# Performance work log

Hardware: AMD Instinct MI355X
Metric: run time of the kernel (lower is better)

## Reference

```python
import jax, jax.numpy as jnp
import numpy as np

EPS = 1e-5
WSZ = 8
DH = 32


def _ln_chan(x, g, b):
    # channel LayerNorm over dim=1 of (B,C,H,W), biased variance
    mu = jnp.mean(x, axis=1, keepdims=True)
    var = jnp.mean((x - mu) ** 2, axis=1, keepdims=True)
    return (x - mu) / jnp.sqrt(var + EPS) * g[None, :, None, None] + b[None, :, None, None]


def _conv_transpose2d(x, w, b, stride, pad):
    # torch ConvTranspose2d: w is (C_in, C_out, kh, kw)
    k = w.shape[2]
    wf = jnp.flip(w, (2, 3)).transpose(1, 0, 2, 3)  # (O, I, kh, kw)
    out = jax.lax.conv_general_dilated(
        x, wf, window_strides=(1, 1),
        padding=[(k - 1 - pad, k - 1 - pad)] * 2,
        lhs_dilation=(stride, stride),
        dimension_numbers=("NCHW", "OIHW", "NCHW"))
    return out + b[None, :, None, None]


def _rope_cs(wh, ww, dh, dtype):
    quarter = dh // 4
    freq = 1.0 / (10000.0 ** (jnp.arange(quarter, dtype=dtype) / quarter))
    th = jnp.arange(wh, dtype=dtype)[:, None] * freq          # (wh, q)
    tw = jnp.arange(ww, dtype=dtype)[:, None] * freq          # (ww, q)
    th = jnp.broadcast_to(th[:, None, :], (wh, ww, quarter)).reshape(wh * ww, quarter)
    tw = jnp.broadcast_to(tw[None, :, :], (wh, ww, quarter)).reshape(wh * ww, quarter)
    theta = jnp.concatenate([th, tw], axis=-1)                # (L, dh/2)
    cos = jnp.concatenate([jnp.cos(theta), jnp.cos(theta)], axis=-1)  # (L, dh)
    sin = jnp.concatenate([jnp.sin(theta), jnp.sin(theta)], axis=-1)
    return cos, sin


def _rot_half(x):
    x1, x2 = jnp.split(x, 2, axis=-1)
    return jnp.concatenate([-x2, x1], axis=-1)


def _attn_block(x, g, b, wqkv, wout, bout, shifted):
    B, C, H, W = x.shape
    heads = C // DH
    xn = _ln_chan(x, g, b)
    if shifted:
        xn = jnp.roll(xn, shift=(-(WSZ // 2), -(WSZ // 2)), axis=(2, 3))
    nh, nw = H // WSZ, W // WSZ
    # window partition: (B,C,H,W) -> (B*nh*nw, L, C), L = WSZ*WSZ
    t = xn.reshape(B, C, nh, WSZ, nw, WSZ).transpose(0, 2, 4, 3, 5, 1)
    t = t.reshape(B * nh * nw, WSZ * WSZ, C)
    qkv = t @ wqkv.T                                           # (Bw, L, 3C)
    q, k, v = jnp.split(qkv, 3, axis=-1)

    def split_heads(a):
        return a.reshape(a.shape[0], a.shape[1], heads, DH).transpose(0, 2, 1, 3)
    q, k, v = map(split_heads, (q, k, v))                      # (Bw, h, L, d)
    cos, sin = _rope_cs(WSZ, WSZ, DH, q.dtype)                 # (L, d)
    q = q * cos + _rot_half(q) * sin
    k = k * cos + _rot_half(k) * sin
    scale = DH ** -0.5
    att = jax.nn.softmax(jnp.einsum("bhid,bhjd->bhij", q * scale, k), axis=-1)
    out = jnp.einsum("bhij,bhjd->bhid", att, v)                # (Bw, h, L, d)
    out = out.transpose(0, 2, 1, 3).reshape(B * nh * nw, WSZ * WSZ, C)
    out = out @ wout.T + bout
    out = out.reshape(B, nh, nw, WSZ, WSZ, C).transpose(0, 5, 1, 3, 2, 4).reshape(B, C, H, W)
    if shifted:
        out = jnp.roll(out, shift=(WSZ // 2, WSZ // 2), axis=(2, 3))
    return out


def _ff(x, g, b, w1, b1, w2, b2):
    xn = _ln_chan(x, g, b)
    h = jnp.einsum("bchw,oc->bohw", xn, w1) + b1[None, :, None, None]
    h = jax.nn.gelu(h)
    return jnp.einsum("bchw,oc->bohw", h, w2) + b2[None, :, None, None]


def _forward(x, ct_w2, ct_b2, ct_w4, ct_b4,
             a1_g, a1_b, a1_wqkv, a1_wout, a1_bout,
             f1_g, f1_b, f1_w1, f1_b1, f1_w2, f1_b2,
             a2_g, a2_b, a2_wqkv, a2_wout, a2_bout,
             f2_g, f2_b, f2_w1, f2_b1, f2_w2, f2_b2):
    # CrossExpandLayer: kernels [2,4], stride 2, padding (k-2)//2
    y2 = _conv_transpose2d(x, ct_w2, ct_b2, stride=2, pad=0)
    y4 = _conv_transpose2d(x, ct_w4, ct_b4, stride=2, pad=1)
    h = jnp.concatenate([y2, y4], axis=1)                      # (B, dim_out, 2H, 2W)
    h = h + _attn_block(h, a1_g, a1_b, a1_wqkv, a1_wout, a1_bout, shifted=False)
    h = h + _ff(h, f1_g, f1_b, f1_w1, f1_b1, f1_w2, f1_b2)
    h = h + _attn_block(h, a2_g, a2_b, a2_wqkv, a2_wout, a2_bout, shifted=True)
    h = h + _ff(h, f2_g, f2_b, f2_w1, f2_b1, f2_w2, f2_b2)
    return h


def setup_inputs() -> dict:
    key = jax.random.key(0)
    ks = jax.random.split(key, 32)
    DIM_IN, DIM = 512, 256
    MULT = 4
    s = 0.02
    inp = {"x": jax.random.normal(ks[0], (2, DIM_IN, 64, 128), dtype=jnp.float32)}
    # CrossExpandLayer: dim_scales = [128, 128]
    inp["ct_w2"] = jax.random.normal(ks[1], (DIM_IN, DIM // 2, 2, 2), jnp.float32) * s
    inp["ct_b2"] = jnp.zeros((DIM // 2,), jnp.float32)
    inp["ct_w4"] = jax.random.normal(ks[2], (DIM_IN, DIM // 2, 4, 4), jnp.float32) * s
    inp["ct_b4"] = jnp.zeros((DIM // 2,), jnp.float32)
    for i, pre in enumerate(["a1", "a2"]):
        inp[pre + "_g"] = jnp.ones((DIM,), jnp.float32)
        inp[pre + "_b"] = jnp.zeros((DIM,), jnp.float32)
        inp[pre + "_wqkv"] = jax.random.normal(ks[3 + 2 * i], (3 * DIM, DIM), jnp.float32) * s
        inp[pre + "_wout"] = jax.random.normal(ks[4 + 2 * i], (DIM, DIM), jnp.float32) * s
        inp[pre + "_bout"] = jnp.zeros((DIM,), jnp.float32)
    for i, pre in enumerate(["f1", "f2"]):
        inp[pre + "_g"] = jnp.ones((DIM,), jnp.float32)
        inp[pre + "_b"] = jnp.zeros((DIM,), jnp.float32)
        inp[pre + "_w1"] = jax.random.normal(ks[10 + 2 * i], (MULT * DIM, DIM), jnp.float32) * s
        inp[pre + "_b1"] = jnp.zeros((MULT * DIM,), jnp.float32)
        inp[pre + "_w2"] = jax.random.normal(ks[11 + 2 * i], (DIM, MULT * DIM), jnp.float32) * s
        inp[pre + "_b2"] = jnp.zeros((DIM,), jnp.float32)
    return inp


def reference(x, ct_w2, ct_b2, ct_w4, ct_b4,
              a1_g, a1_b, a1_wqkv, a1_wout, a1_bout,
              f1_g, f1_b, f1_w1, f1_b1, f1_w2, f1_b2,
              a2_g, a2_b, a2_wqkv, a2_wout, a2_bout,
              f2_g, f2_b, f2_w1, f2_b1, f2_w2, f2_b2):
    return _forward(x, ct_w2, ct_b2, ct_w4, ct_b4,
                    a1_g, a1_b, a1_wqkv, a1_wout, a1_bout,
                    f1_g, f1_b, f1_w1, f1_b1, f1_w2, f1_b2,
                    a2_g, a2_b, a2_wqkv, a2_wout, a2_bout,
                    f2_g, f2_b, f2_w1, f2_b1, f2_w2, f2_b2)
```

## Files before the change

kernel.cpp:

```cpp
#include <hip/hip_runtime.h>
#include <hip/hip_bf16.h>
#include <math.h>

typedef __bf16 bf16_t;
typedef __bf16 bf16x8 __attribute__((ext_vector_type(8)));
typedef float  f32x4 __attribute__((ext_vector_type(4)));

constexpr int B_  = 2;
constexpr int CIN = 512, HI = 64, WI = 128;
constexpr int C_  = 256, H_ = 128, W_ = 256;
constexpr int NTOK = B_ * H_ * W_;
constexpr int NWIN = 1024;

__device__ __forceinline__ unsigned short f2bu(float x) {
    return __builtin_bit_cast(unsigned short, (bf16_t)x);
}

__global__ __launch_bounds__(256) void k_rope(float* __restrict__ rope) {
    int i = blockIdx.x * 256 + threadIdx.x;
    if (i >= 2048) return;
    int l = i >> 5, d = i & 31;
    int j = d & 15;
    int ly = l >> 3, lx = l & 7;
    float fr = powf(10000.f, -(float)(j & 7) / 8.f);
    float t = (j < 8 ? (float)ly : (float)lx) * fr;
    rope[i]        = cosf(t);
    rope[2048 + i] = sinf(t);
}

struct CvtSeg { const float* s; bf16_t* d; unsigned n; };
struct CvtParams { CvtSeg seg[8]; };

__global__ __launch_bounds__(256) void k_cvt(CvtParams P) {
    unsigned base = (blockIdx.x * 256u + threadIdx.x) * 4u;
    for (int s = 0; s < 8; s++) {
        unsigned n = P.seg[s].n;
        if (base < n) {
            float4 v = *(const float4*)(P.seg[s].s + base);
            ushort4 o;
            o.x = f2bu(v.x); o.y = f2bu(v.y); o.z = f2bu(v.z); o.w = f2bu(v.w);
            *(ushort4*)(P.seg[s].d + base) = o;
            return;
        }
        base -= n;
    }
}

__global__ __launch_bounds__(256) void k_trx(const float* __restrict__ x,
                                             bf16_t* __restrict__ xT) {
    __shared__ float t[64][65];
    int pos0 = blockIdx.x << 6;
    int ci0  = blockIdx.y << 6;
    int b    = blockIdx.z;
    int tid = threadIdx.x;
    int cpos = tid & 63, rb = tid >> 6;
    const float* src = x + ((size_t)(b * CIN + ci0) << 13) + pos0;
    #pragma unroll
    for (int i = 0; i < 16; i++) {
        int ci = rb + (i << 2);
        t[ci][cpos] = src[((size_t)ci << 13) + cpos];
    }
    __syncthreads();
    int row = tid >> 2, q = tid & 3;
    bf16_t* dst = xT + ((size_t)((b << 13) + pos0 + row) << 9) + ci0 + (q << 4);
    union { uint4 u[2]; unsigned short us[16]; } o;
    #pragma unroll
    for (int e = 0; e < 16; e++)
        o.us[e] = f2bu(t[(q << 4) + e][row]);
    *(uint4*)dst = o.u[0];
    *(uint4*)(dst + 8) = o.u[1];
}

__global__ __launch_bounds__(256) void k_bmat(const float* __restrict__ w2,
                                              const float* __restrict__ w4,
                                              const float* __restrict__ cb2,
                                              const float* __restrict__ cb4,
                                              bf16_t* __restrict__ B512,
                                              bf16_t* __restrict__ B2048,
                                              float* __restrict__ cbias) {
    int idx = blockIdx.x * 256 + threadIdx.x;
    if (idx < 262144) {
        int ci = idx & 511, o = (idx >> 9) & 127, p = idx >> 16;
        int rp = p >> 1, rq = p & 1;
        B512[idx] = (bf16_t)w2[((ci * 128 + o) * 2 + rp) * 2 + rq];
        if (idx < 256) cbias[idx] = idx < 128 ? cb2[idx] : cb4[idx - 128];
    } else {
        int i4 = idx - 262144;
        int k = i4 & 2047, o2 = (i4 >> 11) & 127, p = i4 >> 18;
        int ci = k & 511, t = k >> 9;
        int rp = p >> 1, rq = p & 1, a = t >> 1, c = t & 1;
        int kh = 3 - rp - 2 * a, kw = 3 - rq - 2 * c;
        B2048[i4] = (bf16_t)w4[((ci * 128 + o2) * 4 + kh) * 4 + kw];
    }
}

__device__ __forceinline__ int winmap_pos(int idx, int shift) {
    int win = idx >> 6, l = idx & 63;
    int b = win >> 9, wy = (win >> 5) & 15, wx = win & 31;
    int y = ((wy << 3) + (l >> 3) + shift) & 127;
    int x = ((wx << 3) + (l & 7) + shift) & 255;
    return (b << 15) + (y << 8) + x;
}

__device__ __forceinline__ float gelu_tanh(float x) {
    float u = 1.5957691216057308f * (x + 0.044715f * x * x * x);
    return x - x * __builtin_amdgcn_rcpf(__expf(u) + 1.f);
}

__device__ __forceinline__ int swz(int row, int byteoff) {
    return (row << 7) + (byteoff ^ ((row & 7) << 4));
}

template<int MODE>
__device__ __forceinline__ void gemm_body(
    char* smem,
    const bf16_t* __restrict__ A, const bf16_t* __restrict__ Bw,
    const float* __restrict__ bias, bf16_t* __restrict__ Cb,
    float* __restrict__ Hres, const float* __restrict__ rope,
    int K, int ldc, int pshift, int colbase)
{
    char* Asb = smem;
    char* Bsb = smem + 16384;
    const int tid = threadIdx.x;

    int gx = gridDim.x;
    int bx = blockIdx.x, by = blockIdx.y;
    if ((gridDim.y & 7) == 0) {
        int lin = by * gx + bx;
        int grp = gx << 3;
        int q = lin / grp, r = lin - q * grp;
        by = (r & 7) + (q << 3);
        bx = r >> 3;
    }
    const int m0 = by << 7, n0 = bx << 7;

    const int w = tid >> 6, l = tid & 63;
    const int wm = (w >> 1) << 6, wn = (w & 1) << 6;
    const int r16 = l & 15, r4 = l >> 4;
    const int arow = tid >> 3, abyte = (tid & 7) << 4;

    const bf16_t* Ag = A + (size_t)(m0 + arow) * K + ((tid & 7) << 3);
    const bf16_t* Bg = Bw + (size_t)(n0 + arow) * K + ((tid & 7) << 3);

    f32x4 acc[4][4] = {};
    uint4 ra[4], rb[4];
    #pragma unroll
    for (int i = 0; i < 4; i++) {
        ra[i] = *(const uint4*)(Ag + (size_t)(i << 5) * K);
        rb[i] = *(const uint4*)(Bg + (size_t)(i << 5) * K);
    }
    for (int kt = 0; kt < K; kt += 64) {
        __syncthreads();
        #pragma unroll
        for (int i = 0; i < 4; i++) {
            *(uint4*)(Asb + swz(arow + (i << 5), abyte)) = ra[i];
            *(uint4*)(Bsb + swz(arow + (i << 5), abyte)) = rb[i];
        }
        __syncthreads();
        if (kt + 64 < K) {
            #pragma unroll
            for (int i = 0; i < 4; i++) {
                ra[i] = *(const uint4*)(Ag + (size_t)(i << 5) * K + kt + 64);
                rb[i] = *(const uint4*)(Bg + (size_t)(i << 5) * K + kt + 64);
            }
        }
        #pragma unroll
        for (int kk = 0; kk < 2; kk++) {
            bf16x8 af[4], bfr[4];
            #pragma unroll
            for (int f = 0; f < 4; f++)
                af[f] = *(const bf16x8*)(Asb + swz(wm + (f << 4) + r16, (kk << 6) + (r4 << 4)));
            #pragma unroll
            for (int f = 0; f < 4; f++)
                bfr[f] = *(const bf16x8*)(Bsb + swz(wn + (f << 4) + r16, (kk << 6) + (r4 << 4)));
            #pragma unroll
            for (int fm = 0; fm < 4; fm++)
                #pragma unroll
                for (int fn = 0; fn < 4; fn++)
                    acc[fm][fn] = __builtin_amdgcn_mfma_f32_16x16x32_bf16(
                        af[fm], bfr[fn], acc[fm][fn], 0, 0, 0);
        }
    }

    float* Lt = (float*)smem;
    const int wgrp = wn >> 6;
    #pragma unroll
    for (int p2 = 0; p2 < 2; p2++) {
        __syncthreads();
        if (wgrp == p2) {
            #pragma unroll
            for (int fm = 0; fm < 4; fm++) {
                int lrow = wm + (fm << 4) + (r4 << 2);
                #pragma unroll
                for (int fn = 0; fn < 4; fn++) {
                    f32x4 v = acc[fm][fn];
                    int lcol = (fn << 4) + r16;
                    #pragma unroll
                    for (int j = 0; j < 4; j++)
                        Lt[(lrow + j) * 72 + lcol] = v[j];
                }
            }
        }
        __syncthreads();
        if constexpr (MODE == 0) {
            const int c0 = (tid & 7) << 3;
            const int gcol = n0 + (p2 << 6) + c0;
            const int which = gcol >> 8;
            const int dbase = c0 & 31;
            const int pc = c0 ^ 16;
            const float sc = (which == 0) ? 0.17677669529663687f : 1.f;
            #pragma unroll
            for (int rnd = 0; rnd < 4; rnd++) {
                int row = (tid >> 3) + (rnd << 5);
                int lidx = (m0 + row) & 63;
                float vv[8];
                *(float4*)(vv)     = *(const float4*)(Lt + row * 72 + c0);
                *(float4*)(vv + 4) = *(const float4*)(Lt + row * 72 + c0 + 4);
                union { uint4 q; unsigned short us[8]; } o;
                if (which < 2) {
                    float pp[8];
                    *(float4*)(pp)     = *(const float4*)(Lt + row * 72 + pc);
                    *(float4*)(pp + 4) = *(const float4*)(Lt + row * 72 + pc + 4);
                    #pragma unroll
                    for (int i = 0; i < 8; i++) {
                        int d = dbase + i;
                        float cs = rope[lidx * 32 + d];
                        float sn = rope[2048 + lidx * 32 + d];
                        float rot = (d < 16) ? -pp[i] : pp[i];
                        o.us[i] = f2bu((vv[i] * cs + rot * sn) * sc);
                    }
                } else {
                    #pragma unroll
                    for (int i = 0; i < 8; i++) o.us[i] = f2bu(vv[i]);
                }
                *(uint4*)(Cb + (size_t)(m0 + row) * ldc + gcol) = o.q;
            }
        } else {
            const int c0 = (tid & 15) << 2;
            const int gcol = colbase + n0 + (p2 << 6) + c0;
            float bb[4];
            *(float4*)bb = *(const float4*)(bias + gcol);
            const int rp = pshift >> 1, rq = pshift & 1;
            #pragma unroll
            for (int rnd = 0; rnd < 8; rnd++) {
                int row = (tid >> 4) + (rnd << 4);
                float4 v = *(const float4*)(Lt + row * 72 + c0);
                int idx = m0 + row;
                int b = idx >> 13, u = (idx >> 7) & 63, vpos = idx & 127;
                int pos = (b << 15) + (((u << 1) + rp) << 8) + (vpos << 1) + rq;
                float* hp = Hres + ((size_t)pos << 8) + gcol;
                float4 r2;
                r2.x = v.x + bb[0]; r2.y = v.y + bb[1];
                r2.z = v.z + bb[2]; r2.w = v.w + bb[3];
                *(float4*)hp = r2;
            }
        }
    }
}

__device__ __forceinline__ void conv4_body(
    char* smem, const bf16_t* __restrict__ xT,
    const bf16_t* __restrict__ B2048, const float* __restrict__ cbias,
    float* __restrict__ h_t, int par)
{
    char* Asb = smem;
    char* Bsb = smem + 16384;
    const int tid = threadIdx.x;
    const int rp = par >> 1, rq = par & 1;
    const int m0 = blockIdx.y << 7;

    const int w = tid >> 6, l = tid & 63;
    const int wm = (w >> 1) << 6, wn = (w & 1) << 6;
    const int r16 = l & 15, r4 = l >> 4;
    const int arow = tid >> 3, abyte = (tid & 7) << 4;
    const int klane = (tid & 7) << 3;

    int mr_[4], u_[4], v_[4];
    #pragma unroll
    for (int i = 0; i < 4; i++) {
        mr_[i] = m0 + arow + (i << 5);
        u_[i] = (mr_[i] >> 7) & 63;
        v_[i] = mr_[i] & 127;
    }
    const bf16_t* Bp = B2048 + ((size_t)par << 18);

    auto loadA = [&](int c, uint4* r) {
        int t = c >> 3, ci0 = (c & 7) << 6;
        int dh = rp - 1 + (t >> 1), dw = rq - 1 + (t & 1);
        int off = (dh << 7) + dw;
        #pragma unroll
        for (int i = 0; i < 4; i++) {
            bool ok = ((unsigned)(u_[i] + dh) < (unsigned)HI) &&
                      ((unsigned)(v_[i] + dw) < (unsigned)WI);
            if (ok)
                r[i] = *(const uint4*)(xT + ((size_t)(mr_[i] + off) << 9) + ci0 + klane);
            else
                r[i] = uint4{0, 0, 0, 0};
        }
    };
    auto loadB = [&](int c, uint4* r) {
        #pragma unroll
        for (int i = 0; i < 4; i++)
            r[i] = *(const uint4*)(Bp + ((size_t)(arow + (i << 5)) << 11)
                                   + (c << 6) + klane);
    };

    f32x4 acc[4][4] = {};
    uint4 ra[4], rb[4];
    loadA(0, ra);
    loadB(0, rb);
    for (int c = 0; c < 32; c++) {
        __syncthreads();
        #pragma unroll
        for (int i = 0; i < 4; i++) {
            *(uint4*)(Asb + swz(arow + (i << 5), abyte)) = ra[i];
            *(uint4*)(Bsb + swz(arow + (i << 5), abyte)) = rb[i];
        }
        __syncthreads();
        if (c + 1 < 32) {
            loadA(c + 1, ra);
            loadB(c + 1, rb);
        }
        #pragma unroll
        for (int kk = 0; kk < 2; kk++) {
            bf16x8 af[4], bfr[4];
            #pragma unroll
            for (int f = 0; f < 4; f++)
                af[f] = *(const bf16x8*)(Asb + swz(wm + (f << 4) + r16, (kk << 6) + (r4 << 4)));
            #pragma unroll
            for (int f = 0; f < 4; f++)
                bfr[f] = *(const bf16x8*)(Bsb + swz(wn + (f << 4) + r16, (kk << 6) + (r4 << 4)));
            #pragma unroll
            for (int fm = 0; fm < 4; fm++)
                #pragma unroll
                for (int fn = 0; fn < 4; fn++)
                    acc[fm][fn] = __builtin_amdgcn_mfma_f32_16x16x32_bf16(
                        af[fm], bfr[fn], acc[fm][fn], 0, 0, 0);
        }
    }

    float* Lt = (float*)smem;
    const int wgrp = wn >> 6;
    #pragma unroll
    for (int p2 = 0; p2 < 2; p2++) {
        __syncthreads();
        if (wgrp == p2) {
            #pragma unroll
            for (int fm = 0; fm < 4; fm++) {
                int lrow = wm + (fm << 4) + (r4 << 2);
                #pragma unroll
                for (int fn = 0; fn < 4; fn++) {
                    f32x4 v = acc[fm][fn];
                    int lcol = (fn << 4) + r16;
                    #pragma unroll
                    for (int j = 0; j < 4; j++)
                        Lt[(lrow + j) * 72 + lcol] = v[j];
                }
            }
        }
        __syncthreads();
        const int c0 = (tid & 15) << 2;
        const int gcol = 128 + (p2 << 6) + c0;
        float bb[4];
        *(float4*)bb = *(const float4*)(cbias + gcol);
        #pragma unroll
        for (int rnd = 0; rnd < 8; rnd++) {
            int row = (tid >> 4) + (rnd << 4);
            float4 v = *(const float4*)(Lt + row * 72 + c0);
            int idx = m0 + row;
            int b = idx >> 13, u = (idx >> 7) & 63, vpos = idx & 127;
            int pos = (b << 15) + (((u << 1) + rp) << 8) + (vpos << 1) + rq;
            float* hp = h_t + ((size_t)pos << 8) + gcol;
            float4 r2;
            r2.x = v.x + bb[0]; r2.y = v.y + bb[1];
            r2.z = v.z + bb[2]; r2.w = v.w + bb[3];
            *(float4*)hp = r2;
        }
    }
}

__global__ __launch_bounds__(256) void k_qkv_gemm(
    const bf16_t* __restrict__ A, const bf16_t* __restrict__ Bw,
    bf16_t* __restrict__ Cb, const float* __restrict__ rope, int K, int ldc) {
    __shared__ char smem[36864];
    gemm_body<0>(smem, A, Bw, nullptr, Cb, nullptr, rope, K, ldc, 0, 0);
}

__global__ __launch_bounds__(256) void k_conv(
    const bf16_t* __restrict__ xT, const bf16_t* __restrict__ B512,
    const bf16_t* __restrict__ B2048, const float* __restrict__ cbias,
    float* __restrict__ h_t) {
    __shared__ char smem[36864];
    int z = blockIdx.z;
    if (z < 4) {
        gemm_body<4>(smem, xT, B512 + ((size_t)z << 16), cbias, nullptr,
                     h_t, nullptr, 512, 0, z, 0);
    } else {
        conv4_body(smem, xT, B2048, cbias, h_t, z - 4);
    }
}

__global__ __launch_bounds__(256) void k_attnp(const bf16_t* __restrict__ qkv,
                                               const bf16_t* __restrict__ wout,
                                               const float* __restrict__ bout,
                                               float* __restrict__ h_t,
                                               int win_base, int shift) {
    __shared__ char smem[18944];
    bf16_t* Vs = (bf16_t*)smem;
    const int tid = threadIdx.x;
    const int w = tid >> 6, l = tid & 63;
    const int r16 = l & 15, r4 = l >> 4;
    bf16_t* Ps = (bf16_t*)(smem + 4608) + w * 1152;
    bf16_t* Os = (bf16_t*)(smem + 13824) + w * 640;
    const int winl = blockIdx.x;
    const bf16_t* qb = qkv + ((size_t)winl << 6) * 768;

    f32x4 acc[16] = {};
    for (int h = 0; h < 8; h++) {
        const int ho = h << 5;
        __syncthreads();
        {
            int tok = tid >> 2, dq = (tid & 3) << 3;
            bf16x8 vv = *(const bf16x8*)(qb + tok * 768 + 512 + ho + dq);
            #pragma unroll
            for (int e = 0; e < 8; e++)
                Vs[(dq + e) * 68 + tok] = vv[e];
        }
        __syncthreads();
        bf16x8 qa = *(const bf16x8*)(qb + (w * 16 + r16) * 768 + ho + r4 * 8);
        f32x4 s[4];
        #pragma unroll
        for (int jt = 0; jt < 4; jt++) {
            f32x4 z = {};
            bf16x8 kb = *(const bf16x8*)(qb + (jt * 16 + r16) * 768 + 256 + ho + r4 * 8);
            s[jt] = __builtin_amdgcn_mfma_f32_16x16x32_bf16(qa, kb, z, 0, 0, 0);
        }
        #pragma unroll
        for (int j = 0; j < 4; j++) {
            float m = fmaxf(fmaxf(s[0][j], s[1][j]), fmaxf(s[2][j], s[3][j]));
            #pragma unroll
            for (int o = 8; o > 0; o >>= 1) m = fmaxf(m, __shfl_xor(m, o));
            float sum = 0.f;
            #pragma unroll
            for (int jt = 0; jt < 4; jt++) { s[jt][j] = __expf(s[jt][j] - m); sum += s[jt][j]; }
            #pragma unroll
            for (int o = 8; o > 0; o >>= 1) sum += __shfl_xor(sum, o);
            float inv = 1.f / sum;
            #pragma unroll
            for (int jt = 0; jt < 4; jt++)
                Ps[(r4 * 4 + j) * 72 + jt * 16 + r16] = (bf16_t)(s[jt][j] * inv);
        }
        f32x4 ov[2] = {};
        #pragma unroll
        for (int kt = 0; kt < 2; kt++) {
            bf16x8 pa = *(const bf16x8*)(Ps + r16 * 72 + kt * 32 + r4 * 8);
            #pragma unroll
            for (int nt = 0; nt < 2; nt++) {
                bf16x8 vb = *(const bf16x8*)(Vs + (nt * 16 + r16) * 68 + kt * 32 + r4 * 8);
                ov[nt] = __builtin_amdgcn_mfma_f32_16x16x32_bf16(pa, vb, ov[nt], 0, 0, 0);
            }
        }
        #pragma unroll
        for (int nt = 0; nt < 2; nt++)
            #pragma unroll
            for (int j = 0; j < 4; j++)
                Os[(r4 * 4 + j) * 40 + nt * 16 + r16] = (bf16_t)ov[nt][j];
        bf16x8 oa = *(const bf16x8*)(Os + r16 * 40 + r4 * 8);
        #pragma unroll
        for (int nt = 0; nt < 16; nt++) {
            bf16x8 wb = *(const bf16x8*)(wout + (nt * 16 + r16) * 256 + ho + r4 * 8);
            acc[nt] = __builtin_amdgcn_mfma_f32_16x16x32_bf16(oa, wb, acc[nt], 0, 0, 0);
        }
    }

    float* Lt = (float*)smem;
    const int gwin = win_base + winl;
    #pragma unroll
    for (int p = 0; p < 4; p++) {
        __syncthreads();
        #pragma unroll
        for (int t2 = 0; t2 < 4; t2++) {
            f32x4 v = acc[p * 4 + t2];
            #pragma unroll
            for (int j = 0; j < 4; j++)
                Lt[(w * 16 + r4 * 4 + j) * 68 + t2 * 16 + r16] = v[j];
        }
        __syncthreads();
        int row = tid >> 2, c0 = (tid & 3) << 4;
        int pos = winmap_pos((gwin << 6) + row, shift);
        float* hp = h_t + ((size_t)pos << 8) + (p << 6) + c0;
        const float* bp = bout + (p << 6) + c0;
        #pragma unroll
        for (int i = 0; i < 4; i++) {
            float4 v = *(const float4*)(Lt + row * 68 + c0 + (i << 2));
            float4 bb = *(const float4*)(bp + (i << 2));
            float4 r = *(const float4*)(hp + (i << 2));
            r.x += v.x + bb.x; r.y += v.y + bb.y;
            r.z += v.z + bb.z; r.w += v.w + bb.w;
            *(float4*)(hp + (i << 2)) = r;
        }
    }
}

__global__ __launch_bounds__(512, 4) void k_ffn(const float* __restrict__ h_in,
                                                const float* __restrict__ gam,
                                                const float* __restrict__ bet,
                                                const bf16_t* __restrict__ w1,
                                                const float* __restrict__ b1,
                                                const bf16_t* __restrict__ w2,
                                                const float* __restrict__ b2,
                                                float* __restrict__ h_t) {
    __shared__ char smem[65536];
    bf16_t* Xs = (bf16_t*)smem;
    bf16_t* Hs = (bf16_t*)(smem + 32768);
    const int tid = threadIdx.x;
    const int w = tid >> 6, l = tid & 63;
    const int r16 = l & 15, r4 = l >> 4;
    const int tok0 = blockIdx.x << 6;

    {
        const int c = l << 2;
        float4 gv = *(const float4*)(gam + c);
        float4 bv = *(const float4*)(bet + c);
        const float* hsrc = h_in + ((size_t)tok0 << 8);
        #pragma unroll
        for (int rep = 0; rep < 8; rep++) {
            int row = (rep << 3) + w;
            float4 v = *(const float4*)(hsrc + ((size_t)row << 8) + c);
            float s  = v.x + v.y + v.z + v.w;
            float s2 = v.x * v.x + v.y * v.y + v.z * v.z + v.w * v.w;
            #pragma unroll
            for (int o = 32; o > 0; o >>= 1) {
                s += __shfl_xor(s, o); s2 += __shfl_xor(s2, o);
            }
            float mu = s * (1.f / 256.f);
            float rs = rsqrtf(s2 * (1.f / 256.f) - mu * mu + 1e-5f);
            ushort4 o4;
            o4.x = f2bu((v.x - mu) * rs * gv.x + bv.x);
            o4.y = f2bu((v.y - mu) * rs * gv.y + bv.y);
            o4.z = f2bu((v.z - mu) * rs * gv.z + bv.z);
            o4.w = f2bu((v.w - mu) * rs * gv.w + bv.w);
            *(ushort4*)(Xs + (row << 8) + (c ^ ((row & 7) << 3))) = o4;
        }
    }
    __syncthreads();

    f32x4 acc2[4][2] = {};
    #pragma unroll
    for (int hc2 = 0; hc2 < 4; hc2++) {
        f32x4 acc1[4] = {};
        #pragma unroll
        for (int kk = 0; kk < 8; kk++) {
            bf16x8 af[4];
            #pragma unroll
            for (int fm = 0; fm < 4; fm++)
                af[fm] = *(const bf16x8*)(Xs + (((fm << 4) + r16) << 8)
                          + (((kk << 5) + (r4 << 3)) ^ ((r16 & 7) << 3)));
            int nh = (hc2 << 8) + (w << 4) + r16;
            bf16x8 b1f = *(const bf16x8*)(w1 + ((size_t)nh << 8) + (kk << 5) + (r4 << 3));
            #pragma unroll
            for (int fm = 0; fm < 4; fm++)
                acc1[fm] = __builtin_amdgcn_mfma_f32_16x16x32_bf16(
                    af[fm], b1f, acc1[fm], 0, 0, 0);
        }
        if (hc2) __syncthreads();
        {
            int hcol = (w << 4) + r16;
            float bi = b1[(hc2 << 8) + hcol];
            #pragma unroll
            for (int fm = 0; fm < 4; fm++)
                #pragma unroll
                for (int j = 0; j < 4; j++) {
                    int row = (fm << 4) + (r4 << 2) + j;
                    Hs[(row << 8) + (hcol ^ ((row & 7) << 3))] =
                        (bf16_t)gelu_tanh(acc1[fm][j] + bi);
                }
        }
        #pragma unroll
        for (int fm = 0; fm < 4; fm++) acc1[fm] = f32x4{};
        #pragma unroll
        for (int kk = 0; kk < 8; kk++) {
            bf16x8 af[4];
            #pragma unroll
            for (int fm = 0; fm < 4; fm++)
                af[fm] = *(const bf16x8*)(Xs + (((fm << 4) + r16) << 8)
                          + (((kk << 5) + (r4 << 3)) ^ ((r16 & 7) << 3)));
            int nh = (hc2 << 8) + 128 + (w << 4) + r16;
            bf16x8 b1f = *(const bf16x8*)(w1 + ((size_t)nh << 8) + (kk << 5) + (r4 << 3));
            #pragma unroll
            for (int fm = 0; fm < 4; fm++)
                acc1[fm] = __builtin_amdgcn_mfma_f32_16x16x32_bf16(
                    af[fm], b1f, acc1[fm], 0, 0, 0);
        }
        {
            int hcol = 128 + (w << 4) + r16;
            float bi = b1[(hc2 << 8) + hcol];
            #pragma unroll
            for (int fm = 0; fm < 4; fm++)
                #pragma unroll
                for (int j = 0; j < 4; j++) {
                    int row = (fm << 4) + (r4 << 2) + j;
                    Hs[(row << 8) + (hcol ^ ((row & 7) << 3))] =
                        (bf16_t)gelu_tanh(acc1[fm][j] + bi);
                }
        }
        __syncthreads();
        #pragma unroll
        for (int kk = 0; kk < 8; kk++) {
            bf16x8 a2[4];
            #pragma unroll
            for (int fm = 0; fm < 4; fm++)
                a2[fm] = *(const bf16x8*)(Hs + (((fm << 4) + r16) << 8)
                          + (((kk << 5) + (r4 << 3)) ^ ((r16 & 7) << 3)));
            bf16x8 b2f[2];
            #pragma unroll
            for (int fn = 0; fn < 2; fn++) {
                int nc = (w << 5) + (fn << 4) + r16;
                b2f[fn] = *(const bf16x8*)(w2 + ((size_t)nc << 10) + (hc2 << 8)
                           + (kk << 5) + (r4 << 3));
            }
            #pragma unroll
            for (int fm = 0; fm < 4; fm++)
                #pragma unroll
                for (int fn = 0; fn < 2; fn++)
                    acc2[fm][fn] = __builtin_amdgcn_mfma_f32_16x16x32_bf16(
                        a2[fm], b2f[fn], acc2[fm][fn], 0, 0, 0);
        }
    }

    float* Lt = (float*)smem;
    #pragma unroll
    for (int p = 0; p < 2; p++) {
        __syncthreads();
        if ((w >> 2) == p) {
            #pragma unroll
            for (int fm = 0; fm < 4; fm++)
                #pragma unroll
                for (int fn = 0; fn < 2; fn++) {
                    f32x4 v = acc2[fm][fn];
                    int col = ((w & 3) << 5) + (fn << 4) + r16;
                    #pragma unroll
                    for (int j = 0; j < 4; j++)
                        Lt[((fm << 4) + (r4 << 2) + j) * 132 + col] = v[j];
                }
        }
        __syncthreads();
        int row = tid >> 3;
        int c0 = (tid & 7) << 4;
        float* hp = h_t + (((size_t)(tok0 + row)) << 8) + (p << 7) + c0;
        const float* bp = b2 + (p << 7) + c0;
        #pragma unroll
        for (int i = 0; i < 4; i++) {
            float4 v = *(const float4*)(Lt + row * 132 + c0 + (i << 2));
            float4 bb = *(const float4*)(bp + (i << 2));
            float4 r = *(const float4*)(hp + (i << 2));
            r.x += v.x + bb.x; r.y += v.y + bb.y;
            r.z += v.z + bb.z; r.w += v.w + bb.w;
            *(float4*)(hp + (i << 2)) = r;
        }
    }
}

__global__ __launch_bounds__(256) void k_ln(const float* __restrict__ h,
                                            const float* __restrict__ g,
                                            const float* __restrict__ bt,
                                            bf16_t* __restrict__ xn,
                                            int windowed, int shift) {
    int tok = (blockIdx.x << 2) + (threadIdx.x >> 6);
    int l = threadIdx.x & 63;
    float4 v = *(const float4*)(h + ((size_t)tok << 8) + (l << 2));
    float s  = v.x + v.y + v.z + v.w;
    float s2 = v.x * v.x + v.y * v.y + v.z * v.z + v.w * v.w;
    #pragma unroll
    for (int o = 32; o > 0; o >>= 1) { s += __shfl_xor(s, o); s2 += __shfl_xor(s2, o); }
    float mu = s * (1.f / 256.f);
    float rs = rsqrtf(s2 * (1.f / 256.f) - mu * mu + 1e-5f);
    int orow = tok;
    if (windowed) {
        int b = tok >> 15, img = tok & 32767;
        int y2 = ((img >> 8) - shift) & 127;
        int x2 = ((img & 255) - shift) & 255;
        orow = (((b << 9) + ((y2 >> 3) << 5) + (x2 >> 3)) << 6) + ((y2 & 7) << 3) + (x2 & 7);
    }
    int c = l << 2;
    float4 gv = *(const float4*)(g + c);
    float4 bv = *(const float4*)(bt + c);
    ushort4 o;
    o.x = f2bu((v.x - mu) * rs * gv.x + bv.x);
    o.y = f2bu((v.y - mu) * rs * gv.y + bv.y);
    o.z = f2bu((v.z - mu) * rs * gv.z + bv.z);
    o.w = f2bu((v.w - mu) * rs * gv.w + bv.w);
    *(ushort4*)(xn + ((size_t)orow << 8) + c) = o;
}

__global__ __launch_bounds__(256) void k_tr(const float* __restrict__ src,
                                            float* __restrict__ dst) {
    __shared__ float t[64][65];
    int tx = blockIdx.x & 3;
    int ty = blockIdx.x >> 2;
    int tid = threadIdx.x;
    int c = (tx << 6) + (tid & 63), r = tid >> 6;
    #pragma unroll
    for (int i = 0; i < 16; i++)
        t[r + i * 4][tid & 63] = src[(size_t)((ty << 6) + r + i * 4) * 256 + c];
    __syncthreads();
    int tok = (ty << 6) + (tid & 63);
    int c2 = tid >> 6;
    #pragma unroll
    for (int i = 0; i < 16; i++)
        dst[(size_t)((tx << 6) + c2 + i * 4) * 32768 + tok] = t[tid & 63][c2 + i * 4];
}

__global__ __launch_bounds__(256) void k_tr2(const float* __restrict__ ht,
                                             float* __restrict__ out) {
    __shared__ float t[128][65];
    int tk0 = blockIdx.x << 7;
    int c0  = blockIdx.y << 6;
    int tid = threadIdx.x;
    #pragma unroll
    for (int rep = 0; rep < 8; rep++) {
        int idx = rep * 256 + tid;
        int row = idx >> 4, c4 = (idx & 15) << 2;
        float4 v = *(const float4*)(ht + ((size_t)(tk0 + row) << 8) + c0 + c4);
        t[row][c4] = v.x; t[row][c4 + 1] = v.y; t[row][c4 + 2] = v.z; t[row][c4 + 3] = v.w;
    }
    __syncthreads();
    int b = tk0 >> 15, img0 = tk0 & 32767;
    #pragma unroll
    for (int rep = 0; rep < 8; rep++) {
        int idx = rep * 256 + tid;
        int jc = idx & 31, c = idx >> 5;
        float4 v;
        v.x = t[(jc << 2) + 0][c];
        v.y = t[(jc << 2) + 1][c];
        v.z = t[(jc << 2) + 2][c];
        v.w = t[(jc << 2) + 3][c];
        *(float4*)(out + (((size_t)(b << 8) + c0 + c) << 15) + img0 + (jc << 2)) = v;
    }
}

extern "C" void kernel_launch(void* const* d_in, const int* in_sizes, int n_in,
                              void* d_out, int out_size, void* d_ws, size_t ws_size,
                              hipStream_t stream) {
    const float* x     = (const float*)d_in[0];
    const float* ct_w2 = (const float*)d_in[1];
    const float* ct_b2 = (const float*)d_in[2];
    const float* ct_w4 = (const float*)d_in[3];
    const float* ct_b4 = (const float*)d_in[4];
    const float* ag[2]  = {(const float*)d_in[5],  (const float*)d_in[10]};
    const float* abt[2] = {(const float*)d_in[6],  (const float*)d_in[11]};
    const float* awq[2] = {(const float*)d_in[7],  (const float*)d_in[12]};
    const float* awo[2] = {(const float*)d_in[8],  (const float*)d_in[13]};
    const float* abo[2] = {(const float*)d_in[9],  (const float*)d_in[14]};
    const float* fg[2]  = {(const float*)d_in[15], (const float*)d_in[21]};
    const float* fbt[2] = {(const float*)d_in[16], (const float*)d_in[22]};
    const float* fw1[2] = {(const float*)d_in[17], (const float*)d_in[23]};
    const float* fb1[2] = {(const float*)d_in[18], (const float*)d_in[24]};
    const float* fw2[2] = {(const float*)d_in[19], (const float*)d_in[25]};
    const float* fb2[2] = {(const float*)d_in[20], (const float*)d_in[26]};

    char* w = (char*)d_ws;
    auto alloc = [&](size_t bytes) {
        char* p = w; w += (bytes + 255) & ~(size_t)255; return p;
    };
    float*  rope  = (float*)alloc(4096 * 4);
    bf16_t* wqkvb[2] = {(bf16_t*)alloc(196608 * 2), (bf16_t*)alloc(196608 * 2)};
    bf16_t* woutb[2] = {(bf16_t*)alloc(65536 * 2),  (bf16_t*)alloc(65536 * 2)};
    bf16_t* fw1b[2]  = {(bf16_t*)alloc(262144 * 2), (bf16_t*)alloc(262144 * 2)};
    bf16_t* fw2b[2]  = {(bf16_t*)alloc(262144 * 2), (bf16_t*)alloc(262144 * 2)};
    bf16_t* B512  = (bf16_t*)alloc((size_t)262144 * 2);
    bf16_t* B2048 = (bf16_t*)alloc((size_t)1048576 * 2);
    float*  cbias = (float*)alloc(256 * 4);
    bf16_t* xT    = (bf16_t*)alloc((size_t)16384 * 512 * 2);
    char*   XN    = alloc(33554432);
    bf16_t* xn = (bf16_t*)XN;

    size_t usedB = (size_t)(w - (char*)d_ws);
    size_t rem = ws_size > usedB ? ws_size - usedB : 0;
    const size_t HT_BYTES = (size_t)NTOK * C_ * 4;
    bool pathA = rem >= HT_BYTES + (size_t)16777216;
    float* h_t = pathA ? (float*)alloc(HT_BYTES) : (float*)d_out;

    usedB = (size_t)(w - (char*)d_ws);
    size_t Sb = ws_size > usedB ? ws_size - usedB : 0;
    if (Sb > (size_t)134217728) Sb = 134217728;
    char* S = w;

    auto p2f = [](size_t v) -> size_t { size_t r = 1; while ((r << 1) <= v) r <<= 1; return r; };
    int CW = (int)(Sb / 98304 >= 1024 ? 1024 : p2f(Sb / 98304));
    if (CW < 16) CW = 16;

    k_rope<<<8, 256, 0, stream>>>(rope);
    CvtParams P;
    P.seg[0] = { awq[0],  wqkvb[0],  196608 };
    P.seg[1] = { awq[1],  wqkvb[1],  196608 };
    P.seg[2] = { awo[0],  woutb[0],  65536 };
    P.seg[3] = { awo[1],  woutb[1],  65536 };
    P.seg[4] = { fw1[0],  fw1b[0],   262144 };
    P.seg[5] = { fw1[1],  fw1b[1],   262144 };
    P.seg[6] = { fw2[0],  fw2b[0],   262144 };
    P.seg[7] = { fw2[1],  fw2b[1],   262144 };
    unsigned total4 = (196608u * 2 + 65536u * 2 + 262144u * 4) / 4;
    k_cvt<<<(total4 + 255) / 256, 256, 0, stream>>>(P);
    k_bmat<<<5120, 256, 0, stream>>>(ct_w2, ct_w4, ct_b2, ct_b4, B512, B2048, cbias);
    k_trx<<<dim3(128, 8, 2), 256, 0, stream>>>(x, xT);

    k_conv<<<dim3(1, 128, 8), 256, 0, stream>>>(xT, B512, B2048, cbias, h_t);

    for (int blk = 0; blk < 2; blk++) {
        int shift = blk ? 4 : 0;
        k_ln<<<NTOK / 4, 256, 0, stream>>>(h_t, ag[blk], abt[blk], xn, 1, shift);
        for (int w0 = 0; w0 < NWIN; w0 += CW) {
            bf16_t* qkvc = (bf16_t*)S;
            k_qkv_gemm<<<dim3(6, CW / 2), 256, 0, stream>>>(
                xn + (size_t)w0 * 64 * 256, wqkvb[blk], qkvc, rope, 256, 768);
            k_attnp<<<CW, 256, 0, stream>>>(qkvc, woutb[blk], abo[blk], h_t, w0, shift);
        }
        k_ffn<<<NTOK / 64, 512, 0, stream>>>(h_t, fg[blk], fbt[blk],
                                             fw1b[blk], fb1[blk],
                                             fw2b[blk], fb2[blk], h_t);
    }

    if (pathA) {
        k_tr2<<<dim3(512, 4), 256, 0, stream>>>(h_t, (float*)d_out);
    } else {
        for (int b = 0; b < 2; b++) {
            hipMemcpyAsync(XN, h_t + (size_t)b * 32768 * 256, 33554432,
                           hipMemcpyDeviceToDevice, stream);
            k_tr<<<2048, 256, 0, stream>>>((const float*)XN,
                                           (float*)d_out + (size_t)b * 256 * 32768);
        }
    }
}
```

Before: 982.0 us.

## Shrink FFN block tile to 32 tokens with 256 threads and regrid warps

Re-tiles the fused FFN kernel so each block handles 32 tokens with 4 warps instead of 64 tokens with 8 warps, halving shared memory per block. The first GEMM now runs in four passes per hidden chunk, and the second GEMM gives each warp 2x4 MFMA fragments instead of 4x2. The aim is smaller blocks, more resident blocks and a larger grid for better occupancy and load balance. In exchange, the full w1/w2 weights are streamed once per 32 tokens rather than per 64, doubling weight reads from cache.

```diff
diff --git a/kernel.cpp b/kernel.cpp
--- a/kernel.cpp
+++ b/kernel.cpp
@@ -502,7 +502,7 @@
     }
 }
 
-__global__ __launch_bounds__(512, 4) void k_ffn(const float* __restrict__ h_in,
+__global__ __launch_bounds__(256, 4) void k_ffn(const float* __restrict__ h_in,
                                                 const float* __restrict__ gam,
                                                 const float* __restrict__ bet,
                                                 const bf16_t* __restrict__ w1,
@@ -510,13 +510,13 @@
                                                 const bf16_t* __restrict__ w2,
                                                 const float* __restrict__ b2,
                                                 float* __restrict__ h_t) {
-    __shared__ char smem[65536];
+    __shared__ char smem[32768];
     bf16_t* Xs = (bf16_t*)smem;
-    bf16_t* Hs = (bf16_t*)(smem + 32768);
+    bf16_t* Hs = (bf16_t*)(smem + 16384);
     const int tid = threadIdx.x;
     const int w = tid >> 6, l = tid & 63;
     const int r16 = l & 15, r4 = l >> 4;
-    const int tok0 = blockIdx.x << 6;
+    const int tok0 = blockIdx.x << 5;
 
     {
         const int c = l << 2;
@@ -525,7 +525,7 @@
         const float* hsrc = h_in + ((size_t)tok0 << 8);
         #pragma unroll
         for (int rep = 0; rep < 8; rep++) {
-            int row = (rep << 3) + w;
+            int row = (rep << 2) + w;
             float4 v = *(const float4*)(hsrc + ((size_t)row << 8) + c);
             float s  = v.x + v.y + v.z + v.w;
             float s2 = v.x * v.x + v.y * v.y + v.z * v.z + v.w * v.w;
@@ -545,84 +545,59 @@
     }
     __syncthreads();
 
-    f32x4 acc2[4][2] = {};
+    f32x4 acc2[2][4] = {};
     #pragma unroll
     for (int hc2 = 0; hc2 < 4; hc2++) {
-        f32x4 acc1[4] = {};
+        #pragma unroll
+        for (int pass = 0; pass < 4; pass++) {
+            f32x4 acc1[2] = {};
+            #pragma unroll
+            for (int kk = 0; kk < 8; kk++) {
+                bf16x8 af[2];
+                #pragma unroll
+                for (int fm = 0; fm < 2; fm++)
+                    af[fm] = *(const bf16x8*)(Xs + (((fm << 4) + r16) << 8)
+                              + (((kk << 5) + (r4 << 3)) ^ ((r16 & 7) << 3)));
+                int nh = (hc2 << 8) + (pass << 6) + (w << 4) + r16;
+                bf16x8 b1f = *(const bf16x8*)(w1 + ((size_t)nh << 8) + (kk << 5) + (r4 << 3));
+                #pragma unroll
+                for (int fm = 0; fm < 2; fm++)
+                    acc1[fm] = __builtin_amdgcn_mfma_f32_16x16x32_bf16(
+                        af[fm], b1f, acc1[fm], 0, 0, 0);
+            }
+            if (hc2 && pass == 0) __syncthreads();
+            {
+                int hcol = (pass << 6) + (w << 4) + r16;
+                float bi = b1[(hc2 << 8) + hcol];
+                #pragma unroll
+                for (int fm = 0; fm < 2; fm++)
+                    #pragma unroll
+                    for (int j = 0; j < 4; j++) {
+                        int row = (fm << 4) + (r4 << 2) + j;
+                        Hs[(row << 8) + (hcol ^ ((row & 7) << 3))] =
+                            (bf16_t)gelu_tanh(acc1[fm][j] + bi);
+                    }
+            }
+        }
+        __syncthreads();
         #pragma unroll
         for (int kk = 0; kk < 8; kk++) {
-            bf16x8 af[4];
-            #pragma unroll
-            for (int fm = 0; fm < 4; fm++)
-                af[fm] = *(const bf16x8*)(Xs + (((fm << 4) + r16) << 8)
-                          + (((kk << 5) + (r4 << 3)) ^ ((r16 & 7) << 3)));
-            int nh = (hc2 << 8) + (w << 4) + r16;
-            bf16x8 b1f = *(const bf16x8*)(w1 + ((size_t)nh << 8) + (kk << 5) + (r4 << 3));
-            #pragma unroll
-            for (int fm = 0; fm < 4; fm++)
-                acc1[fm] = __builtin_amdgcn_mfma_f32_16x16x32_bf16(
-                    af[fm], b1f, acc1[fm], 0, 0, 0);
-        }
-        if (hc2) __syncthreads();
-        {
-            int hcol = (w << 4) + r16;
-            float bi = b1[(hc2 << 8) + hcol];
-            #pragma unroll
-            for (int fm = 0; fm < 4; fm++)
-                #pragma unroll
-                for (int j = 0; j < 4; j++) {
-                    int row = (fm << 4) + (r4 << 2) + j;
-                    Hs[(row << 8) + (hcol ^ ((row & 7) << 3))] =
-                        (bf16_t)gelu_tanh(acc1[fm][j] + bi);
-                }
-        }
-        #pragma unroll
-        for (int fm = 0; fm < 4; fm++) acc1[fm] = f32x4{};
-        #pragma unroll
-        for (int kk = 0; kk < 8; kk++) {
-            bf16x8 af[4];
-            #pragma unroll
-            for (int fm = 0; fm < 4; fm++)
-                af[fm] = *(const bf16x8*)(Xs + (((fm << 4) + r16) << 8)
-                          + (((kk << 5) + (r4 << 3)) ^ ((r16 & 7) << 3)));
-            int nh = (hc2 << 8) + 128 + (w << 4) + r16;
-            bf16x8 b1f = *(const bf16x8*)(w1 + ((size_t)nh << 8) + (kk << 5) + (r4 << 3));
-            #pragma unroll
-            for (int fm = 0; fm < 4; fm++)
-                acc1[fm] = __builtin_amdgcn_mfma_f32_16x16x32_bf16(
-                    af[fm], b1f, acc1[fm], 0, 0, 0);
-        }
-        {
-            int hcol = 128 + (w << 4) + r16;
-            float bi = b1[(hc2 << 8) + hcol];
-            #pragma unroll
-            for (int fm = 0; fm < 4; fm++)
-                #pragma unroll
-                for (int j = 0; j < 4; j++) {
-                    int row = (fm << 4) + (r4 << 2) + j;
-                    Hs[(row << 8) + (hcol ^ ((row & 7) << 3))] =
-                        (bf16_t)gelu_tanh(acc1[fm][j] + bi);
-                }
-        }
-        __syncthreads();
-        #pragma unroll
-        for (int kk = 0; kk < 8; kk++) {
-            bf16x8 a2[4];
-            #pragma unroll
-            for (int fm = 0; fm < 4; fm++)
+            bf16x8 a2[2];
+            #pragma unroll
+            for (int fm = 0; fm < 2; fm++)
                 a2[fm] = *(const bf16x8*)(Hs + (((fm << 4) + r16) << 8)
                           + (((kk << 5) + (r4 << 3)) ^ ((r16 & 7) << 3)));
-            bf16x8 b2f[2];
-            #pragma unroll
-            for (int fn = 0; fn < 2; fn++) {
-                int nc = (w << 5) + (fn << 4) + r16;
+            bf16x8 b2f[4];
+            #pragma unroll
+            for (int fn = 0; fn < 4; fn++) {
+                int nc = (w << 6) + (fn << 4) + r16;
                 b2f[fn] = *(const bf16x8*)(w2 + ((size_t)nc << 10) + (hc2 << 8)
                            + (kk << 5) + (r4 << 3));
             }
             #pragma unroll
-            for (int fm = 0; fm < 4; fm++)
+            for (int fm = 0; fm < 2; fm++)
                 #pragma unroll
-                for (int fn = 0; fn < 2; fn++)
+                for (int fn = 0; fn < 4; fn++)
                     acc2[fm][fn] = __builtin_amdgcn_mfma_f32_16x16x32_bf16(
                         a2[fm], b2f[fn], acc2[fm][fn], 0, 0, 0);
         }
@@ -632,13 +607,13 @@
     #pragma unroll
     for (int p = 0; p < 2; p++) {
         __syncthreads();
-        if ((w >> 2) == p) {
-            #pragma unroll
-            for (int fm = 0; fm < 4; fm++)
+        if ((w >> 1) == p) {
+            #pragma unroll
+            for (int fm = 0; fm < 2; fm++)
                 #pragma unroll
-                for (int fn = 0; fn < 2; fn++) {
+                for (int fn = 0; fn < 4; fn++) {
                     f32x4 v = acc2[fm][fn];
-                    int col = ((w & 3) << 5) + (fn << 4) + r16;
+                    int col = ((w & 1) << 6) + (fn << 4) + r16;
                     #pragma unroll
                     for (int j = 0; j < 4; j++)
                         Lt[((fm << 4) + (r4 << 2) + j) * 132 + col] = v[j];
@@ -816,7 +791,7 @@
                 xn + (size_t)w0 * 64 * 256, wqkvb[blk], qkvc, rope, 256, 768);
             k_attnp<<<CW, 256, 0, stream>>>(qkvc, woutb[blk], abo[blk], h_t, w0, shift);
         }
-        k_ffn<<<NTOK / 64, 512, 0, stream>>>(h_t, fg[blk], fbt[blk],
+        k_ffn<<<NTOK / 32, 256, 0, stream>>>(h_t, fg[blk], fbt[blk],
                                              fw1b[blk], fb1[blk],
                                              fw2b[blk], fb2[blk], h_t);
     }
```

Result: slower. 1.174 ms (+19.6%).
